# Kernel optimization log

Hardware: AMD Instinct MI355X
Metric: run time of the kernel (lower is better)

The kernel has to match this reference:

```python
import jax, jax.numpy as jnp
import numpy as np
import math

DIM = 384
NH = 6
DH = DIM // NH
B = 2
S = 2048
EPS = 1e-6
LN_EPS = 1e-5


def setup_inputs() -> dict:
    key = jax.random.key(0)
    ks = jax.random.split(key, 8)
    q = jax.random.normal(ks[0], (B, S, DIM), dtype=jnp.float32)
    k = jax.random.normal(ks[1], (B, S, DIM), dtype=jnp.float32)
    v = jax.random.normal(ks[2], (B, S, DIM), dtype=jnp.float32)
    # gate linear params (Linear(3*dim, num_heads)); small random weights to exercise the math
    igate_w = jax.random.normal(ks[3], (NH, 3 * DIM), dtype=jnp.float32) * 0.02
    igate_b = jax.random.normal(ks[4], (NH,), dtype=jnp.float32) * 0.1
    fgate_w = jax.random.normal(ks[5], (NH, 3 * DIM), dtype=jnp.float32) * 0.02
    fgate_b = jnp.linspace(3.0, 6.0, NH, dtype=jnp.float32)
    # MultiHeadLayerNorm residual weight (stored as delta, effective scale = 1 + w)
    outnorm_weight = jax.random.normal(ks[6], (DIM,), dtype=jnp.float32) * 0.02
    return {"q": q, "k": k, "v": v, "igate_w": igate_w, "igate_b": igate_b,
            "fgate_w": fgate_w, "fgate_b": fgate_b, "outnorm_weight": outnorm_weight}


def _mlstm_forward(q, k, v, igate_w, igate_b, fgate_w, fgate_b, outnorm_weight):
    Bq, Sq, _ = q.shape
    gate_in = jnp.concatenate([q, k, v], axis=-1)                       # (B,S,3D)
    ig = gate_in @ igate_w.T + igate_b                                   # (B,S,NH)
    fg = gate_in @ fgate_w.T + fgate_b                                   # (B,S,NH)
    # split heads: (B,NH,S,DH)
    qh = q.reshape(Bq, Sq, NH, DH).transpose(0, 2, 1, 3)
    kh = k.reshape(Bq, Sq, NH, DH).transpose(0, 2, 1, 3)
    vh = v.reshape(Bq, Sq, NH, DH).transpose(0, 2, 1, 3)
    ig = ig.transpose(0, 2, 1)                                           # (B,NH,S)
    fg = fg.transpose(0, 2, 1)                                           # (B,NH,S)

    log_fg = jax.nn.log_sigmoid(fg)                                      # (B,NH,S)
    lfc = jnp.concatenate([jnp.zeros((Bq, NH, 1), dtype=q.dtype),
                           jnp.cumsum(log_fg, axis=-1)], axis=-1)        # (B,NH,S+1)
    # log_fg_matrix[i,j] = cumsum[i] - cumsum[j] (sliced [1:,1:]), masked causal
    diff = lfc[:, :, 1:, None] - lfc[:, :, None, 1:]                     # (B,NH,S,S)
    ltr = jnp.tril(jnp.ones((Sq, Sq), dtype=bool))
    log_fg_mat = jnp.where(ltr, diff, -jnp.inf)
    log_D = log_fg_mat + ig[:, :, None, :]                               # + igate^T
    max_log_D = jnp.max(log_D, axis=-1, keepdims=True)                   # rowwise stabilize
    D = jnp.exp(log_D - max_log_D)
    qk = jnp.einsum('bhsd,bhtd->bhst', qh, kh) / math.sqrt(DH)
    C = qk * D
    normalizer = jnp.maximum(jnp.abs(jnp.sum(C, axis=-1, keepdims=True)),
                             jnp.exp(-max_log_D))
    h = jnp.einsum('bhst,bhtd->bhsd', C / (normalizer + EPS), vh)        # (B,NH,S,DH)

    # MultiHeadLayerNorm == group_norm over each head's DH channels, scale=(1+w)
    mean = jnp.mean(h, axis=-1, keepdims=True)
    var = jnp.var(h, axis=-1, keepdims=True)
    normed = (h - mean) / jnp.sqrt(var + LN_EPS)
    scale = (1.0 + outnorm_weight).reshape(NH, DH)[None, :, None, :]
    out = normed * scale
    return out.transpose(0, 2, 1, 3).reshape(Bq, Sq, DIM)


def reference(q, k, v, igate_w, igate_b, fgate_w, fgate_b, outnorm_weight):
    return _mlstm_forward(q, k, v, igate_w, igate_b, fgate_w, fgate_b, outnorm_weight)
```

## Files before the change

### kernel.cpp

```cpp
#include <hip/hip_runtime.h>
#include <math.h>

#define DIM 384
#define NH 6
#define DH 64
#define B_ 2
#define S_ 2048
#define EPS 1e-6f
#define LN_EPS 1e-5f
#define G3 (3*DIM)
#define LOG2E 1.44269504f
#define KSTR 72
#define NT (S_/64)
#define NSPLIT 4
#define NBH (B_*NH)

typedef __attribute__((ext_vector_type(8))) short bf16x8;
typedef __attribute__((ext_vector_type(4))) short bf16x4;
typedef __attribute__((ext_vector_type(4))) float f32x4;

__device__ __forceinline__ unsigned short f2bf(float f){
    unsigned int u = __float_as_uint(f);
    u += 0x7fff + ((u >> 16) & 1);
    return (unsigned short)(u >> 16);
}

__device__ __forceinline__ float logsig(float x){
    return fminf(x, 0.f) - log1pf(expf(-fabsf(x)));
}

__global__ __launch_bounds__(256) void gates_kernel(
    const float* __restrict__ q, const float* __restrict__ k, const float* __restrict__ v,
    const float* __restrict__ iw, const float* __restrict__ ib,
    const float* __restrict__ fw, const float* __restrict__ fb,
    float* __restrict__ ig_out, float* __restrict__ lf_out) {
    int wave = (blockIdx.x * 256 + threadIdx.x) >> 6;
    int lane = threadIdx.x & 63;
    int b = wave / S_, s = wave % S_;
    size_t base = ((size_t)b * S_ + s) * DIM;
    float aI[NH], aF[NH];
    #pragma unroll
    for (int h = 0; h < NH; h++){ aI[h] = 0.f; aF[h] = 0.f; }
    for (int g = lane; g < G3/4; g += 64) {
        int e = g * 4;
        float4 x4;
        if (e < DIM)        x4 = *(const float4*)(q + base + e);
        else if (e < 2*DIM) x4 = *(const float4*)(k + base + e - DIM);
        else                x4 = *(const float4*)(v + base + e - 2*DIM);
        #pragma unroll
        for (int h = 0; h < NH; h++){
            float4 wi = *(const float4*)(iw + h*G3 + e);
            float4 wf = *(const float4*)(fw + h*G3 + e);
            aI[h] = fmaf(x4.x, wi.x, fmaf(x4.y, wi.y, fmaf(x4.z, wi.z, fmaf(x4.w, wi.w, aI[h]))));
            aF[h] = fmaf(x4.x, wf.x, fmaf(x4.y, wf.y, fmaf(x4.z, wf.z, fmaf(x4.w, wf.w, aF[h]))));
        }
    }
    #pragma unroll
    for (int h = 0; h < NH; h++){
        #pragma unroll
        for (int off = 32; off >= 1; off >>= 1){
            aI[h] += __shfl_xor(aI[h], off, 64);
            aF[h] += __shfl_xor(aF[h], off, 64);
        }
    }
    if (lane == 0) {
        #pragma unroll
        for (int h = 0; h < NH; h++){
            ig_out[((size_t)b*NH + h)*S_ + s] = aI[h] + ib[h];
            lf_out[((size_t)b*NH + h)*S_ + s] = logsig(aF[h] + fb[h]);
        }
    }
}

__global__ __launch_bounds__(256) void scan_kernel(const float* __restrict__ lf,
                                                   float* __restrict__ cum){
    int bh = blockIdx.x;
    const float* src = lf + (size_t)bh * S_;
    float* dst = cum + (size_t)bh * S_;
    int tid = threadIdx.x;
    float loc[8];
    float run = 0.f;
    #pragma unroll
    for (int j = 0; j < 8; j++){ run += src[tid*8 + j]; loc[j] = run; }
    __shared__ float sm[256];
    sm[tid] = run;
    __syncthreads();
    float total = run;
    for (int off = 1; off < 256; off <<= 1){
        float vv = (tid >= off) ? sm[tid - off] : 0.f;
        __syncthreads();
        sm[tid] += vv;
        __syncthreads();
    }
    float excl = sm[tid] - total;
    #pragma unroll
    for (int j = 0; j < 8; j++) dst[tid*8 + j] = excl + loc[j];
}

__global__ __launch_bounds__(256) void mlstm_part(
    const float* __restrict__ q, const float* __restrict__ k, const float* __restrict__ v,
    const float* __restrict__ ig, const float* __restrict__ cum,
    float* __restrict__ pO, float* __restrict__ pM, float* __restrict__ pL) {
    int lin = blockIdx.x;
    int sp  = lin / NBH;
    int bh  = lin % NBH;
    int st  = (NT - 1) - (sp >> 2);
    int c   = sp & 3;
    int L   = (st + 4) >> 2;
    int tb0 = c * L;
    int tb1 = min((c + 1) * L, st + 1);
    int pblk = lin;
    int tid = threadIdx.x;

    if (tb0 >= tb1){
        if (tid < 64){ pM[pblk*64 + tid] = -INFINITY; pL[pblk*64 + tid] = 0.f; }
        return;
    }

    __shared__ unsigned short kt[64*KSTR];
    __shared__ unsigned short vt[64*KSTR];
    __shared__ float cumL[64];
    __shared__ float igL[64];

    int b = bh / NH, h = bh % NH;
    int s0 = st * 64;
    int wv   = tid >> 6;
    int lane = tid & 63;
    int lq   = lane & 15;
    int quad = lane >> 4;

    const float* qbase = q + (size_t)b*S_*DIM + h*DH;
    const float* kbase = k + (size_t)b*S_*DIM + h*DH;
    const float* vbase = v + (size_t)b*S_*DIM + h*DH;
    const float* igb = ig + (size_t)bh*S_;
    const float* cmb = cum + (size_t)bh*S_;

    int s_glob = s0 + 16*wv + lq;

    bf16x8 qf[2];
    {
        const float* qr = qbase + (size_t)s_glob*DIM;
        #pragma unroll
        for (int ks = 0; ks < 2; ks++){
            float4 a = *(const float4*)(qr + 32*ks + 8*quad);
            float4 cc = *(const float4*)(qr + 32*ks + 8*quad + 4);
            bf16x8 t;
            t[0]=(short)f2bf(a.x*0.125f); t[1]=(short)f2bf(a.y*0.125f);
            t[2]=(short)f2bf(a.z*0.125f); t[3]=(short)f2bf(a.w*0.125f);
            t[4]=(short)f2bf(cc.x*0.125f); t[5]=(short)f2bf(cc.y*0.125f);
            t[6]=(short)f2bf(cc.z*0.125f); t[7]=(short)f2bf(cc.w*0.125f);
            qf[ks] = t;
        }
    }

    float cq  = cmb[s_glob];
    float m_s = -INFINITY, b_s = 0.f;
    f32x4 oacc[4];
    #pragma unroll
    for (int cg = 0; cg < 4; cg++) oacc[cg] = (f32x4){0.f,0.f,0.f,0.f};

    int srow[4], scol[4];
    #pragma unroll
    for (int i = 0; i < 4; i++){
        int idx = tid + 256*i;
        srow[i] = idx >> 4;
        scol[i] = (idx & 15) << 2;
    }

    float4 kreg[4], vreg[4];
    {
        const float* kb = kbase + (size_t)(tb0*64)*DIM;
        const float* vb = vbase + (size_t)(tb0*64)*DIM;
        #pragma unroll
        for (int i = 0; i < 4; i++){
            kreg[i] = *(const float4*)(kb + (size_t)srow[i]*DIM + scol[i]);
            vreg[i] = *(const float4*)(vb + (size_t)srow[i]*DIM + scol[i]);
        }
    }

    for (int t0 = tb0*64; t0 < tb1*64; t0 += 64){
        __syncthreads();
        #pragma unroll
        for (int i = 0; i < 4; i++){
            int r = srow[i], cc = scol[i];
            ushort4 kk; kk.x=f2bf(kreg[i].x); kk.y=f2bf(kreg[i].y);
            kk.z=f2bf(kreg[i].z); kk.w=f2bf(kreg[i].w);
            *(ushort4*)&kt[r*KSTR + cc] = kk;
            vt[(cc+0)*KSTR + r] = f2bf(vreg[i].x);
            vt[(cc+1)*KSTR + r] = f2bf(vreg[i].y);
            vt[(cc+2)*KSTR + r] = f2bf(vreg[i].z);
            vt[(cc+3)*KSTR + r] = f2bf(vreg[i].w);
        }
        if (tid < 64){ cumL[tid] = cmb[t0 + tid]; igL[tid] = igb[t0 + tid]; }
        __syncthreads();

        if (t0 + 64 < tb1*64){
            const float* kb = kbase + (size_t)(t0 + 64)*DIM;
            const float* vb = vbase + (size_t)(t0 + 64)*DIM;
            #pragma unroll
            for (int i = 0; i < 4; i++){
                kreg[i] = *(const float4*)(kb + (size_t)srow[i]*DIM + scol[i]);
                vreg[i] = *(const float4*)(vb + (size_t)srow[i]*DIM + scol[i]);
            }
        }

        f32x4 st4[4];
        #pragma unroll
        for (int tb = 0; tb < 4; tb++) st4[tb] = (f32x4){0.f,0.f,0.f,0.f};
        #pragma unroll
        for (int ks = 0; ks < 2; ks++){
            #pragma unroll
            for (int tb = 0; tb < 4; tb++){
                bf16x8 af = *(const bf16x8*)&kt[(16*tb + lq)*KSTR + 32*ks + 8*quad];
                st4[tb] = __builtin_amdgcn_mfma_f32_16x16x32_bf16(af, qf[ks], st4[tb], 0, 0, 0);
            }
        }

        bool diag = (t0 == s0);
        float dv[4][4];
        float pmax = -INFINITY;
        #pragma unroll
        for (int tb = 0; tb < 4; tb++){
            float4 c4 = *(const float4*)&cumL[16*tb + 4*quad];
            float4 g4 = *(const float4*)&igL[16*tb + 4*quad];
            float ccv[4] = {c4.x, c4.y, c4.z, c4.w};
            float gg[4] = {g4.x, g4.y, g4.z, g4.w};
            #pragma unroll
            for (int r = 0; r < 4; r++){
                float d = cq - ccv[r] + gg[r];
                if (diag && (t0 + 16*tb + 4*quad + r) > s_glob) d = -INFINITY;
                dv[tb][r] = d;
                pmax = fmaxf(pmax, d);
            }
        }
        pmax = fmaxf(pmax, __shfl_xor(pmax, 16, 64));
        pmax = fmaxf(pmax, __shfl_xor(pmax, 32, 64));
        float mn = fmaxf(m_s, pmax);
        float sc = exp2f((m_s - mn) * LOG2E);
        m_s = mn;
        float rs = 0.f;
        bf16x4 pf[4];
        #pragma unroll
        for (int tb = 0; tb < 4; tb++){
            #pragma unroll
            for (int r = 0; r < 4; r++){
                float pv = st4[tb][r] * exp2f((dv[tb][r] - mn) * LOG2E);
                rs += pv;
                pf[tb][r] = (short)f2bf(pv);
            }
        }
        rs += __shfl_xor(rs, 16, 64);
        rs += __shfl_xor(rs, 32, 64);
        b_s = b_s * sc + rs;

        #pragma unroll
        for (int r = 0; r < 4; r++){
            float sco = __shfl(sc, 20*quad + r, 64);
            #pragma unroll
            for (int cg = 0; cg < 4; cg++) oacc[cg][r] *= sco;
        }

        #pragma unroll
        for (int tb = 0; tb < 4; tb++){
            #pragma unroll
            for (int cg = 0; cg < 4; cg++){
                bf16x4 vf = *(const bf16x4*)&vt[(16*cg + lq)*KSTR + 16*tb + 4*quad];
                oacc[cg] = __builtin_amdgcn_mfma_f32_16x16x16bf16_1k(pf[tb], vf, oacc[cg], 0, 0, 0);
            }
        }
    }

    float* po = pO + (size_t)pblk * 4096;
    #pragma unroll
    for (int r = 0; r < 4; r++){
        int row = 16*wv + 4*quad + r;
        #pragma unroll
        for (int cg = 0; cg < 4; cg++)
            po[row*64 + 16*cg + lq] = oacc[cg][r];
    }
    if (quad == 0){
        pM[pblk*64 + 16*wv + lq] = m_s;
        pL[pblk*64 + 16*wv + lq] = b_s;
    }
}

__global__ __launch_bounds__(256) void mlstm_combine(
    const float* __restrict__ pO, const float* __restrict__ pM,
    const float* __restrict__ pL, const float* __restrict__ w,
    float* __restrict__ out) {
    int st = blockIdx.x;
    int bh = blockIdx.y;
    int b = bh / NH, h = bh % NH;
    int tid = threadIdx.x;
    int cl = (tid & 15) * 4;
    int rb = tid >> 4;

    int pblk[NSPLIT];
    #pragma unroll
    for (int p = 0; p < NSPLIT; p++)
        pblk[p] = (((NT - 1 - st) << 2) + p) * NBH + bh;

    float4 wv4 = *(const float4*)(w + h*DH + cl);

    #pragma unroll
    for (int pass = 0; pass < 4; pass++){
        int row = pass*16 + rb;
        float mp[NSPLIT], lp[NSPLIT];
        float mmax = -INFINITY;
        #pragma unroll
        for (int p = 0; p < NSPLIT; p++){
            mp[p] = pM[pblk[p]*64 + row];
            lp[p] = pL[pblk[p]*64 + row];
            mmax = fmaxf(mmax, mp[p]);
        }
        float l = 0.f;
        float4 o = {0.f, 0.f, 0.f, 0.f};
        #pragma unroll
        for (int p = 0; p < NSPLIT; p++){
            float wp = exp2f((mp[p] - mmax) * LOG2E);
            l += wp * lp[p];
            float4 t = *(const float4*)(pO + (size_t)pblk[p]*4096 + row*64 + cl);
            o.x += wp*t.x; o.y += wp*t.y; o.z += wp*t.z; o.w += wp*t.w;
        }
        float nrm = fmaxf(fabsf(l), exp2f(-mmax * LOG2E));
        float inv = 1.f / (nrm + EPS);
        float x[4] = {o.x*inv, o.y*inv, o.z*inv, o.w*inv};
        float s1 = x[0]+x[1]+x[2]+x[3];
        float s2 = x[0]*x[0]+x[1]*x[1]+x[2]*x[2]+x[3]*x[3];
        #pragma unroll
        for (int off = 8; off >= 1; off >>= 1){
            s1 += __shfl_xor(s1, off, 64);
            s2 += __shfl_xor(s2, off, 64);
        }
        float mean = s1 * (1.f/64.f);
        float var  = s2 * (1.f/64.f) - mean*mean;
        float rstd = rsqrtf(var + LN_EPS);
        float4 oo;
        oo.x = (x[0]-mean)*rstd*(1.f + wv4.x);
        oo.y = (x[1]-mean)*rstd*(1.f + wv4.y);
        oo.z = (x[2]-mean)*rstd*(1.f + wv4.z);
        oo.w = (x[3]-mean)*rstd*(1.f + wv4.w);
        *(float4*)(out + ((size_t)b*S_ + st*64 + row)*DIM + h*DH + cl) = oo;
    }
}

extern "C" void kernel_launch(void* const* d_in, const int* in_sizes, int n_in,
                              void* d_out, int out_size, void* d_ws, size_t ws_size,
                              hipStream_t stream) {
    const float* q  = (const float*)d_in[0];
    const float* k  = (const float*)d_in[1];
    const float* v  = (const float*)d_in[2];
    const float* iw = (const float*)d_in[3];
    const float* ib = (const float*)d_in[4];
    const float* fw = (const float*)d_in[5];
    const float* fb = (const float*)d_in[6];
    const float* w  = (const float*)d_in[7];
    float* out = (float*)d_out;

    const int nPart = NBH * NT * NSPLIT;
    float* ig  = (float*)d_ws;
    float* lf  = ig  + (size_t)NBH*S_;
    float* cum = lf  + (size_t)NBH*S_;
    float* pM  = cum + (size_t)NBH*S_;
    float* pL  = pM  + (size_t)nPart*64;
    float* pO  = pL  + (size_t)nPart*64;

    gates_kernel<<<B_*S_/4, 256, 0, stream>>>(q, k, v, iw, ib, fw, fb, ig, lf);
    scan_kernel<<<NBH, 256, 0, stream>>>(lf, cum);
    mlstm_part<<<nPart, 256, 0, stream>>>(q, k, v, ig, cum, pO, pM, pL);
    mlstm_combine<<<dim3(NT, NBH), 256, 0, stream>>>(pO, pM, pL, w, out);
}
```

Baseline: 141.5 us.

## Double split-K partitions, store partial outputs in bf16, load gate values directly

Raises the number of key-range splits per query tile from 4 to 8 so more workgroups run in parallel on the causal attention. Partial outputs are stored as bf16 to halve workspace traffic, and the combine step skips empty partitions. Cumulative-gate and input-gate values are read straight from global memory into registers instead of staged through LDS, and the V tile stride changes to reduce bank conflicts. The cost is more partial blocks, a heavier combine pass, and lower precision in the partial sums.

```diff
diff --git a/kernel.cpp b/kernel.cpp
--- a/kernel.cpp
+++ b/kernel.cpp
@@ -11,8 +11,9 @@
 #define G3 (3*DIM)
 #define LOG2E 1.44269504f
 #define KSTR 72
+#define VSTR 68
 #define NT (S_/64)
-#define NSPLIT 4
+#define NSPLIT 8
 #define NBH (B_*NH)
 
 typedef __attribute__((ext_vector_type(8))) short bf16x8;
@@ -23,6 +24,9 @@
     unsigned int u = __float_as_uint(f);
     u += 0x7fff + ((u >> 16) & 1);
     return (unsigned short)(u >> 16);
+}
+__device__ __forceinline__ float bf2f(unsigned short u){
+    return __uint_as_float(((unsigned int)u) << 16);
 }
 
 __device__ __forceinline__ float logsig(float x){
@@ -100,13 +104,13 @@
 __global__ __launch_bounds__(256) void mlstm_part(
     const float* __restrict__ q, const float* __restrict__ k, const float* __restrict__ v,
     const float* __restrict__ ig, const float* __restrict__ cum,
-    float* __restrict__ pO, float* __restrict__ pM, float* __restrict__ pL) {
+    unsigned short* __restrict__ pOb, float* __restrict__ pM, float* __restrict__ pL) {
     int lin = blockIdx.x;
     int sp  = lin / NBH;
     int bh  = lin % NBH;
-    int st  = (NT - 1) - (sp >> 2);
-    int c   = sp & 3;
-    int L   = (st + 4) >> 2;
+    int st  = (NT - 1) - (sp >> 3);
+    int c   = sp & 7;
+    int L   = (st + 8) >> 3;
     int tb0 = c * L;
     int tb1 = min((c + 1) * L, st + 1);
     int pblk = lin;
@@ -118,9 +122,7 @@
     }
 
     __shared__ unsigned short kt[64*KSTR];
-    __shared__ unsigned short vt[64*KSTR];
-    __shared__ float cumL[64];
-    __shared__ float igL[64];
+    __shared__ unsigned short vt[64*VSTR];
 
     int b = bh / NH, h = bh % NH;
     int s0 = st * 64;
@@ -179,6 +181,13 @@
     }
 
     for (int t0 = tb0*64; t0 < tb1*64; t0 += 64){
+        float4 cumc[4], igc[4];
+        #pragma unroll
+        for (int tb = 0; tb < 4; tb++){
+            cumc[tb] = *(const float4*)(cmb + t0 + 16*tb + 4*quad);
+            igc[tb]  = *(const float4*)(igb + t0 + 16*tb + 4*quad);
+        }
+
         __syncthreads();
         #pragma unroll
         for (int i = 0; i < 4; i++){
@@ -186,12 +195,11 @@
             ushort4 kk; kk.x=f2bf(kreg[i].x); kk.y=f2bf(kreg[i].y);
             kk.z=f2bf(kreg[i].z); kk.w=f2bf(kreg[i].w);
             *(ushort4*)&kt[r*KSTR + cc] = kk;
-            vt[(cc+0)*KSTR + r] = f2bf(vreg[i].x);
-            vt[(cc+1)*KSTR + r] = f2bf(vreg[i].y);
-            vt[(cc+2)*KSTR + r] = f2bf(vreg[i].z);
-            vt[(cc+3)*KSTR + r] = f2bf(vreg[i].w);
-        }
-        if (tid < 64){ cumL[tid] = cmb[t0 + tid]; igL[tid] = igb[t0 + tid]; }
+            vt[(cc+0)*VSTR + r] = f2bf(vreg[i].x);
+            vt[(cc+1)*VSTR + r] = f2bf(vreg[i].y);
+            vt[(cc+2)*VSTR + r] = f2bf(vreg[i].z);
+            vt[(cc+3)*VSTR + r] = f2bf(vreg[i].w);
+        }
         __syncthreads();
 
         if (t0 + 64 < tb1*64){
@@ -221,13 +229,9 @@
         float pmax = -INFINITY;
         #pragma unroll
         for (int tb = 0; tb < 4; tb++){
-            float4 c4 = *(const float4*)&cumL[16*tb + 4*quad];
-            float4 g4 = *(const float4*)&igL[16*tb + 4*quad];
-            float ccv[4] = {c4.x, c4.y, c4.z, c4.w};
-            float gg[4] = {g4.x, g4.y, g4.z, g4.w};
             #pragma unroll
             for (int r = 0; r < 4; r++){
-                float d = cq - ccv[r] + gg[r];
+                float d = cq - cumc[tb][r] + igc[tb][r];
                 if (diag && (t0 + 16*tb + 4*quad + r) > s_glob) d = -INFINITY;
                 dv[tb][r] = d;
                 pmax = fmaxf(pmax, d);
@@ -264,19 +268,19 @@
         for (int tb = 0; tb < 4; tb++){
             #pragma unroll
             for (int cg = 0; cg < 4; cg++){
-                bf16x4 vf = *(const bf16x4*)&vt[(16*cg + lq)*KSTR + 16*tb + 4*quad];
+                bf16x4 vf = *(const bf16x4*)&vt[(16*cg + lq)*VSTR + 16*tb + 4*quad];
                 oacc[cg] = __builtin_amdgcn_mfma_f32_16x16x16bf16_1k(pf[tb], vf, oacc[cg], 0, 0, 0);
             }
         }
     }
 
-    float* po = pO + (size_t)pblk * 4096;
+    unsigned short* po = pOb + (size_t)pblk * 4096;
     #pragma unroll
     for (int r = 0; r < 4; r++){
         int row = 16*wv + 4*quad + r;
         #pragma unroll
         for (int cg = 0; cg < 4; cg++)
-            po[row*64 + 16*cg + lq] = oacc[cg][r];
+            po[row*64 + 16*cg + lq] = f2bf(oacc[cg][r]);
     }
     if (quad == 0){
         pM[pblk*64 + 16*wv + lq] = m_s;
@@ -285,7 +289,7 @@
 }
 
 __global__ __launch_bounds__(256) void mlstm_combine(
-    const float* __restrict__ pO, const float* __restrict__ pM,
+    const unsigned short* __restrict__ pOb, const float* __restrict__ pM,
     const float* __restrict__ pL, const float* __restrict__ w,
     float* __restrict__ out) {
     int st = blockIdx.x;
@@ -298,7 +302,7 @@
     int pblk[NSPLIT];
     #pragma unroll
     for (int p = 0; p < NSPLIT; p++)
-        pblk[p] = (((NT - 1 - st) << 2) + p) * NBH + bh;
+        pblk[p] = (((NT - 1 - st) << 3) + p) * NBH + bh;
 
     float4 wv4 = *(const float4*)(w + h*DH + cl);
 
@@ -314,17 +318,20 @@
             mmax = fmaxf(mmax, mp[p]);
         }
         float l = 0.f;
-        float4 o = {0.f, 0.f, 0.f, 0.f};
+        float ox = 0.f, oy = 0.f, oz = 0.f, ow = 0.f;
         #pragma unroll
         for (int p = 0; p < NSPLIT; p++){
-            float wp = exp2f((mp[p] - mmax) * LOG2E);
-            l += wp * lp[p];
-            float4 t = *(const float4*)(pO + (size_t)pblk[p]*4096 + row*64 + cl);
-            o.x += wp*t.x; o.y += wp*t.y; o.z += wp*t.z; o.w += wp*t.w;
+            if (mp[p] != -INFINITY){
+                float wp = exp2f((mp[p] - mmax) * LOG2E);
+                l += wp * lp[p];
+                ushort4 t4 = *(const ushort4*)(pOb + (size_t)pblk[p]*4096 + row*64 + cl);
+                ox += wp*bf2f(t4.x); oy += wp*bf2f(t4.y);
+                oz += wp*bf2f(t4.z); ow += wp*bf2f(t4.w);
+            }
         }
         float nrm = fmaxf(fabsf(l), exp2f(-mmax * LOG2E));
         float inv = 1.f / (nrm + EPS);
-        float x[4] = {o.x*inv, o.y*inv, o.z*inv, o.w*inv};
+        float x[4] = {ox*inv, oy*inv, oz*inv, ow*inv};
         float s1 = x[0]+x[1]+x[2]+x[3];
         float s2 = x[0]*x[0]+x[1]*x[1]+x[2]*x[2]+x[3]*x[3];
         #pragma unroll
@@ -363,10 +370,10 @@
     float* cum = lf  + (size_t)NBH*S_;
     float* pM  = cum + (size_t)NBH*S_;
     float* pL  = pM  + (size_t)nPart*64;
-    float* pO  = pL  + (size_t)nPart*64;
+    unsigned short* pOb = (unsigned short*)(pL + (size_t)nPart*64);
 
     gates_kernel<<<B_*S_/4, 256, 0, stream>>>(q, k, v, iw, ib, fw, fb, ig, lf);
     scan_kernel<<<NBH, 256, 0, stream>>>(lf, cum);
-    mlstm_part<<<nPart, 256, 0, stream>>>(q, k, v, ig, cum, pO, pM, pL);
-    mlstm_combine<<<dim3(NT, NBH), 256, 0, stream>>>(pO, pM, pL, w, out);
-}
+    mlstm_part<<<nPart, 256, 0, stream>>>(q, k, v, ig, cum, pOb, pM, pL);
+    mlstm_combine<<<dim3(NT, NBH), 256, 0, stream>>>(pOb, pM, pL, w, out);
+}
```

Measured after the change: 157.3 us. 11.2% more time.
